# Performance work log

Hardware: AMD Instinct MI355X
Metric: run time of the kernel (lower is better)

The kernel has to match this reference:

```python
import jax, jax.numpy as jnp
import numpy as np

N_HIT = 50000
N_TRUE = 512
N_EDGE = 40000
D = 8
S_B = 1.0
Q_MIN = 0.5


def setup_inputs() -> dict:
    key = jax.random.key(0)
    k_x, k_f, k_y, k_eh, k_ep = jax.random.split(key, 5)
    x = jax.random.normal(k_x, (N_HIT, D), dtype=jnp.float32)
    # f is a sigmoid-like filter output in (0,1); keep away from 1 so atanh is finite
    f = jax.random.uniform(k_f, (N_HIT,), dtype=jnp.float32, minval=0.01, maxval=0.95)
    # y == -1 marks background hits; otherwise an instance id
    y = jax.random.randint(k_y, (N_HIT,), -1, N_TRUE, dtype=jnp.int64)
    e_h = jax.random.randint(k_eh, (N_EDGE,), 0, N_HIT, dtype=jnp.int64)
    e_p = jax.random.randint(k_ep, (N_EDGE,), 0, N_TRUE, dtype=jnp.int64)
    # guarantee every true particle has at least one assigned hit
    e_p = e_p.at[:N_TRUE].set(jnp.arange(N_TRUE, dtype=jnp.int64))
    return {"x": x, "f": f, "y": y, "e_h": e_h, "e_p": e_p}


def reference(x, f, y, e_h, e_p):
    n_hit = x.shape[0]
    fe = f[e_h]  # [n_edge]
    # scatter_max with zero-initialized output: clamp below at 0
    f_centers = jax.ops.segment_max(fe, e_p, num_segments=N_TRUE)
    f_centers = jnp.maximum(f_centers, 0.0)  # [n_true]
    # argmax hit per particle: among edges attaining the segment max, take largest hit id
    is_max = fe == f_centers[e_p]
    centers = jax.ops.segment_max(jnp.where(is_max, e_h, -1), e_p, num_segments=N_TRUE)  # [n_true]

    bkg_mask = y == -1
    n_bkg = bkg_mask.sum().astype(f.dtype)

    b1 = 1.0 - f_centers.sum() / N_TRUE
    b2 = S_B / n_bkg * jnp.where(bkg_mask, f, 0.0).sum()

    q = jnp.square(jnp.arctanh(f)) + Q_MIN  # [n_hit]

    # membership mask m_ik [n_hit, n_true]
    m_ik = jnp.zeros((n_hit, N_TRUE), dtype=bool).at[e_h, e_p].set(True)

    # pairwise squared distances to condensation centers [n_hit, n_true]
    xc = x[centers]  # [n_true, d]
    dist = jnp.sum(jnp.square(x[:, None, :] - xc[None, :, :]), axis=2)

    # attractive inside instance, hinged repulsive outside
    v = jnp.where(m_ik, dist, jnp.clip(1.0 - dist, 0.0))
    v = (jnp.sum(v * q[centers][None, :], axis=1) * q).sum() / n_hit

    return jnp.stack([b1 + b2, v])
```

## Files before the change

### kernel.cpp

```cpp
#include <hip/hip_runtime.h>
#include <math.h>

#define N_HIT  50000
#define N_TRUE 512
#define N_EDGE 40000
#define Q_MIN  0.5f

#define W_CENTERS   512
#define W_SUMFC     1024
#define W_DONE_EDGE 1025
#define W_DONE_MAIN 1026
#define W_VPART     1040
#define W_ZERO_LO   512
#define W_ZERO_HI   1168
#define W_BKGPART   1200
#define W_BKGCNT    1232
#define W_FCPART    2048
#define W_CTAB      16384
#define W_HREC      32768

#define A_EDGE_BLOCKS 16
#define A_BKG_BLOCKS  32
#define A_GRID 49
#define EPB (N_EDGE / A_EDGE_BLOCKS)

#define E_GRID ((N_EDGE + 255) / 256)

#define KSPLIT 16
#define KCH    (N_TRUE / KSPLIT)
#define HPT    4
#define HCHUNK (256 * HPT)
#define NHB    ((N_HIT + HCHUNK - 1) / HCHUNK)
#define D_DENSE (NHB * KSPLIT)
#define D_CORR  16
#define D_GRID  (D_DENSE + D_CORR)

__global__ __launch_bounds__(256) void k_prep(const float* __restrict__ x,
                                              const float* __restrict__ f,
                                              const int* __restrict__ e_h,
                                              const int* __restrict__ e_p,
                                              const int* __restrict__ y,
                                              unsigned* __restrict__ ws) {
    const int b = blockIdx.x, t = threadIdx.x;
    if (b < A_EDGE_BLOCKS) {
        __shared__ unsigned lmax[N_TRUE];
        lmax[t] = 0u; lmax[t + 256] = 0u;
        __syncthreads();
        const int e0 = b * EPB;
        for (int e = e0 + t; e < e0 + EPB; e += 256)
            atomicMax(&lmax[e_p[e]], __float_as_uint(f[e_h[e]]));
        __syncthreads();
        ws[W_FCPART + b * N_TRUE + t]       = lmax[t];
        ws[W_FCPART + b * N_TRUE + t + 256] = lmax[t + 256];
    } else if (b < A_EDGE_BLOCKS + A_BKG_BLOCKS) {
        const int bb = b - A_EDGE_BLOCKS;
        float2* hrec = (float2*)(ws + W_HREC);
        float sf = 0.f, fc = 0.f;
        for (int i = bb * 256 + t; i < N_HIT; i += A_BKG_BLOCKS * 256) {
            const float4* xp = (const float4*)(x + (size_t)i * 8);
            const float4 x0 = xp[0], x1 = xp[1];
            float xi2 = x0.x * x0.x;
            xi2 = fmaf(x0.y, x0.y, xi2); xi2 = fmaf(x0.z, x0.z, xi2);
            xi2 = fmaf(x0.w, x0.w, xi2); xi2 = fmaf(x1.x, x1.x, xi2);
            xi2 = fmaf(x1.y, x1.y, xi2); xi2 = fmaf(x1.z, x1.z, xi2);
            xi2 = fmaf(x1.w, x1.w, xi2);
            const float fi = f[i];
            const float a  = atanhf(fi);
            hrec[i] = make_float2(xi2, fmaf(a, a, Q_MIN));
            if (y[i] == -1) { sf += fi; fc += 1.f; }
        }
        for (int off = 32; off; off >>= 1) {
            sf += __shfl_down(sf, off, 64);
            fc += __shfl_down(fc, off, 64);
        }
        __shared__ float r[8];
        if ((t & 63) == 0) { r[t >> 6] = sf; r[4 + (t >> 6)] = fc; }
        __syncthreads();
        if (t == 0) {
            ((float*)ws)[W_BKGPART + bb] = r[0] + r[1] + r[2] + r[3];
            ((float*)ws)[W_BKGCNT  + bb] = r[4] + r[5] + r[6] + r[7];
        }
    } else {
        for (int w = W_ZERO_LO + t; w < W_ZERO_HI; w += 256) ws[w] = 0u;
    }
}

__global__ __launch_bounds__(256) void k_edge(const float* __restrict__ x,
                                              const float* __restrict__ f,
                                              const int* __restrict__ e_h,
                                              const int* __restrict__ e_p,
                                              unsigned* __restrict__ ws) {
    const int t = threadIdx.x;
    const int e = blockIdx.x * 256 + t;
    if (e < N_EDGE) {
        const int h = e_h[e], p = e_p[e];
        unsigned fm = 0u;
#pragma unroll
        for (int b = 0; b < A_EDGE_BLOCKS; ++b)
            fm = max(fm, ws[W_FCPART + b * N_TRUE + p]);
        if (__float_as_uint(f[h]) == fm)
            atomicMax((int*)ws + W_CENTERS + p, h);
    }
    __syncthreads();
    __shared__ int is_last;
    if (t == 0) {
        __threadfence();
        is_last = (atomicAdd(&ws[W_DONE_EDGE], 1u) == E_GRID - 1);
    }
    __syncthreads();
    if (!is_last) return;

    __threadfence();
    float local = 0.f;
    for (int p = t; p < N_TRUE; p += 256) {
        unsigned fm = 0u;
#pragma unroll
        for (int b = 0; b < A_EDGE_BLOCKS; ++b)
            fm = max(fm, ws[W_FCPART + b * N_TRUE + p]);
        local += __uint_as_float(fm);
        const int c = __hip_atomic_load((int*)ws + W_CENTERS + p,
                                        __ATOMIC_RELAXED, __HIP_MEMORY_SCOPE_AGENT);
        const float4* xp = (const float4*)(x + (size_t)c * 8);
        const float4 x0 = xp[0], x1 = xp[1];
        float ck2 = x0.x * x0.x;
        ck2 = fmaf(x0.y, x0.y, ck2); ck2 = fmaf(x0.z, x0.z, ck2);
        ck2 = fmaf(x0.w, x0.w, ck2); ck2 = fmaf(x1.x, x1.x, ck2);
        ck2 = fmaf(x1.y, x1.y, ck2); ck2 = fmaf(x1.z, x1.z, ck2);
        ck2 = fmaf(x1.w, x1.w, ck2);
        const float a = atanhf(f[c]);
        float* line = (float*)ws + W_CTAB + (size_t)p * 12;
        ((float4*)line)[0] = x0;
        ((float4*)line)[1] = x1;
        line[8] = ck2;
        line[9] = fmaf(a, a, Q_MIN);
    }
    for (int off = 32; off; off >>= 1) local += __shfl_down(local, off, 64);
    __shared__ float r[4];
    if ((t & 63) == 0) r[t >> 6] = local;
    __syncthreads();
    if (t == 0) ((float*)ws)[W_SUMFC] = r[0] + r[1] + r[2] + r[3];
}

__global__ __launch_bounds__(256, 4) void k_main(const float* __restrict__ x,
                                                 const int* __restrict__ e_h,
                                                 const int* __restrict__ e_p,
                                                 unsigned* __restrict__ ws,
                                                 float* __restrict__ out) {
    const int t = threadIdx.x;
    const int b = blockIdx.x;
    const float2* __restrict__ hrec = (const float2*)(ws + W_HREC);
    float vout = 0.f;

    if (b < D_DENSE) {
        const int hb = b >> 4;
        const int kb = b & 15;
        __shared__ float ct[KCH * 12];
        for (int w = t; w < KCH * 12; w += 256)
            ct[w] = ((const float*)ws)[W_CTAB + kb * KCH * 12 + w];
        __syncthreads();

        float4 xr0[HPT], xr1[HPT];
        float  xi2[HPT], qi[HPT], acc[HPT];
#pragma unroll
        for (int j = 0; j < HPT; ++j) {
            const int i = hb * HCHUNK + j * 256 + t;
            const bool valid = (i < N_HIT);
            const int  ic = valid ? i : 0;
            const float4* xp = (const float4*)(x + (size_t)ic * 8);
            xr0[j] = xp[0]; xr1[j] = xp[1];
            const float2 hq = hrec[ic];
            xi2[j] = hq.x;
            qi[j]  = valid ? hq.y : 0.f;
            acc[j] = 0.f;
        }
#pragma unroll
        for (int k2 = 0; k2 < KCH; ++k2) {
            const float4 c0  = *(const float4*)(ct + 12 * k2);
            const float4 c1  = *(const float4*)(ct + 12 * k2 + 4);
            const float  ck2 = ct[12 * k2 + 8];
            const float  qck = ct[12 * k2 + 9];
#pragma unroll
            for (int j = 0; j < HPT; ++j) {
                float dot = xr0[j].x * c0.x;
                dot = fmaf(xr0[j].y, c0.y, dot); dot = fmaf(xr0[j].z, c0.z, dot);
                dot = fmaf(xr0[j].w, c0.w, dot); dot = fmaf(xr1[j].x, c1.x, dot);
                dot = fmaf(xr1[j].y, c1.y, dot); dot = fmaf(xr1[j].z, c1.z, dot);
                dot = fmaf(xr1[j].w, c1.w, dot);
                const float dist = fmaf(-2.f, dot, xi2[j] + ck2);
                const float rep  = fmaxf(1.f - dist, 0.f);
                acc[j] = fmaf(rep, qck, acc[j]);
            }
        }
#pragma unroll
        for (int j = 0; j < HPT; ++j) vout = fmaf(acc[j], qi[j], vout);
    } else {
        const int cb = b - D_DENSE;
        const float* __restrict__ ctab = (const float*)ws + W_CTAB;
        for (int e = cb * 256 + t; e < N_EDGE; e += D_CORR * 256) {
            const int h = e_h[e], p = e_p[e];
            const float2 hq = hrec[h];
            const float4* xp = (const float4*)(x + (size_t)h * 8);
            const float4 a0 = xp[0], a1 = xp[1];
            const float* line = ctab + (size_t)p * 12;
            const float4 c0 = *(const float4*)line;
            const float4 c1 = *(const float4*)(line + 4);
            const float ck2 = line[8], qck = line[9];
            float dot = a0.x * c0.x;
            dot = fmaf(a0.y, c0.y, dot); dot = fmaf(a0.z, c0.z, dot);
            dot = fmaf(a0.w, c0.w, dot); dot = fmaf(a1.x, c1.x, dot);
            dot = fmaf(a1.y, c1.y, dot); dot = fmaf(a1.z, c1.z, dot);
            dot = fmaf(a1.w, c1.w, dot);
            const float dist  = fmaf(-2.f, dot, hq.x + ck2);
            const float hinge = fmaxf(1.f - dist, 0.f);
            vout = fmaf(hq.y * qck, dist - hinge, vout);
        }
    }

    for (int off = 32; off; off >>= 1) vout += __shfl_down(vout, off, 64);
    __shared__ float r[4];
    if ((t & 63) == 0) r[t >> 6] = vout;
    __syncthreads();
    if (t == 0) {
        atomicAdd((float*)ws + W_VPART + (b & 7) * 16, r[0] + r[1] + r[2] + r[3]);
        __threadfence();
        const unsigned c = atomicAdd(&ws[W_DONE_MAIN], 1u);
        if (c == D_GRID - 1) {
            __threadfence();
            float vs = 0.f;
            for (int s = 0; s < 8; ++s)
                vs += atomicAdd((float*)ws + W_VPART + s * 16, 0.0f);
            float sum_bkg = 0.f, nb = 0.f;
            for (int s = 0; s < A_BKG_BLOCKS; ++s) {
                sum_bkg += __hip_atomic_load((const float*)ws + W_BKGPART + s,
                                             __ATOMIC_RELAXED, __HIP_MEMORY_SCOPE_AGENT);
                nb      += __hip_atomic_load((const float*)ws + W_BKGCNT + s,
                                             __ATOMIC_RELAXED, __HIP_MEMORY_SCOPE_AGENT);
            }
            const float sum_fc = __hip_atomic_load((const float*)ws + W_SUMFC,
                                                   __ATOMIC_RELAXED, __HIP_MEMORY_SCOPE_AGENT);
            out[0] = (1.f - sum_fc / (float)N_TRUE) + sum_bkg / nb;
            out[1] = vs / (float)N_HIT;
        }
    }
}

extern "C" void kernel_launch(void* const* d_in, const int* in_sizes, int n_in,
                              void* d_out, int out_size, void* d_ws, size_t ws_size,
                              hipStream_t stream) {
    const float* x   = (const float*)d_in[0];
    const float* f   = (const float*)d_in[1];
    const int*   y   = (const int*)d_in[2];
    const int*   e_h = (const int*)d_in[3];
    const int*   e_p = (const int*)d_in[4];
    float* out = (float*)d_out;
    unsigned* ws = (unsigned*)d_ws;

    k_prep<<<A_GRID, 256, 0, stream>>>(x, f, e_h, e_p, y, ws);
    k_edge<<<E_GRID, 256, 0, stream>>>(x, f, e_h, e_p, ws);
    k_main<<<D_GRID, 256, 0, stream>>>(x, e_h, e_p, ws, out);
}
```

Measured before the change: 104.9 us.

## Fuse prep, edge and main kernels into one persistent kernel with grid barrier

Replaces the three-kernel pipeline with a tiny init kernel plus one fused kernel of 800 blocks. The segment max and argmax are computed in one pass by packing the float bits and the hit id into a 64-bit atomicMax. The prep phase is separated from the dense phase by a software grid barrier that spins on an arrival counter. The aim is to remove kernel launch gaps and the separate argmax pass, but the barrier only works if all 800 blocks are resident at once, and the edge correction now gathers center data per edge from x and hrec.

Result: slower. 263.3 us (+150.9%).

```diff
diff --git a/kernel.cpp b/kernel.cpp
--- a/kernel.cpp
+++ b/kernel.cpp
@@ -6,57 +6,50 @@
 #define N_EDGE 40000
 #define Q_MIN  0.5f
 
-#define W_CENTERS   512
-#define W_SUMFC     1024
-#define W_DONE_EDGE 1025
-#define W_DONE_MAIN 1026
-#define W_VPART     1040
-#define W_ZERO_LO   512
-#define W_ZERO_HI   1168
-#define W_BKGPART   1200
-#define W_BKGCNT    1232
-#define W_FCPART    2048
-#define W_CTAB      16384
-#define W_HREC      32768
-
-#define A_EDGE_BLOCKS 16
-#define A_BKG_BLOCKS  32
-#define A_GRID 49
-#define EPB (N_EDGE / A_EDGE_BLOCKS)
-
-#define E_GRID ((N_EDGE + 255) / 256)
-
-#define KSPLIT 16
-#define KCH    (N_TRUE / KSPLIT)
-#define HPT    4
-#define HCHUNK (256 * HPT)
-#define NHB    ((N_HIT + HCHUNK - 1) / HCHUNK)
-#define D_DENSE (NHB * KSPLIT)
-#define D_CORR  16
-#define D_GRID  (D_DENSE + D_CORR)
-
-__global__ __launch_bounds__(256) void k_prep(const float* __restrict__ x,
-                                              const float* __restrict__ f,
-                                              const int* __restrict__ e_h,
-                                              const int* __restrict__ e_p,
-                                              const int* __restrict__ y,
-                                              unsigned* __restrict__ ws) {
-    const int b = blockIdx.x, t = threadIdx.x;
-    if (b < A_EDGE_BLOCKS) {
-        __shared__ unsigned lmax[N_TRUE];
-        lmax[t] = 0u; lmax[t + 256] = 0u;
-        __syncthreads();
-        const int e0 = b * EPB;
-        for (int e = e0 + t; e < e0 + EPB; e += 256)
-            atomicMax(&lmax[e_p[e]], __float_as_uint(f[e_h[e]]));
-        __syncthreads();
-        ws[W_FCPART + b * N_TRUE + t]       = lmax[t];
-        ws[W_FCPART + b * N_TRUE + t + 256] = lmax[t + 256];
-    } else if (b < A_EDGE_BLOCKS + A_BKG_BLOCKS) {
-        const int bb = b - A_EDGE_BLOCKS;
-        float2* hrec = (float2*)(ws + W_HREC);
-        float sf = 0.f, fc = 0.f;
-        for (int i = bb * 256 + t; i < N_HIT; i += A_BKG_BLOCKS * 256) {
+#define W_SEG     0
+#define W_ARRIVE  1024
+#define W_DONE    1025
+#define W_SUMFC   1026
+#define W_SUMBKG  1027
+#define W_NBKG    1028
+#define W_VPART   1040
+#define W_ZERO_HI 1168
+#define W_HREC    2048
+
+#define G_BLOCKS  800
+#define EPB       (N_EDGE / G_BLOCKS)
+#define KSPLIT    16
+#define KCH       (N_TRUE / KSPLIT)
+#define HPT       4
+#define HCHUNK    (256 * HPT)
+
+__global__ __launch_bounds__(256) void k_init(unsigned* __restrict__ ws) {
+    for (int w = threadIdx.x; w < W_ZERO_HI; w += 256) ws[w] = 0u;
+}
+
+__global__ __launch_bounds__(256, 4) void k_fused(const float* __restrict__ x,
+                                                  const float* __restrict__ f,
+                                                  const int* __restrict__ y,
+                                                  const int* __restrict__ e_h,
+                                                  const int* __restrict__ e_p,
+                                                  unsigned* __restrict__ ws,
+                                                  float* __restrict__ out) {
+    const int t = threadIdx.x, b = blockIdx.x;
+    unsigned long long* __restrict__ seg = (unsigned long long*)ws;
+    float2* __restrict__ hrec = (float2*)(ws + W_HREC);
+
+    if (t >= 64 && t < 64 + EPB) {
+        const int e = b * EPB + (t - 64);
+        const int h = e_h[e], p = e_p[e];
+        const unsigned long long packed =
+            ((unsigned long long)__float_as_uint(f[h]) << 32) | (unsigned)h;
+        atomicMax(&seg[p], packed);
+    }
+    if (t < 64) {
+        const int i = b * 64 + t;
+        float sf = 0.f;
+        bool isb = false;
+        if (i < N_HIT) {
             const float4* xp = (const float4*)(x + (size_t)i * 8);
             const float4 x0 = xp[0], x1 = xp[1];
             float xi2 = x0.x * x0.x;
@@ -67,178 +60,127 @@
             const float fi = f[i];
             const float a  = atanhf(fi);
             hrec[i] = make_float2(xi2, fmaf(a, a, Q_MIN));
-            if (y[i] == -1) { sf += fi; fc += 1.f; }
-        }
-        for (int off = 32; off; off >>= 1) {
-            sf += __shfl_down(sf, off, 64);
-            fc += __shfl_down(fc, off, 64);
-        }
-        __shared__ float r[8];
-        if ((t & 63) == 0) { r[t >> 6] = sf; r[4 + (t >> 6)] = fc; }
+            isb = (y[i] == -1);
+            if (isb) sf = fi;
+        }
+        for (int off = 32; off; off >>= 1) sf += __shfl_down(sf, off, 64);
+        const unsigned long long bal = __ballot(isb);
+        if (t == 0) {
+            atomicAdd((float*)ws + W_SUMBKG, sf);
+            atomicAdd(&ws[W_NBKG], (unsigned)__popcll(bal));
+        }
+    }
+
+    __threadfence();
+    __syncthreads();
+    if (t == 0) {
+        atomicAdd(&ws[W_ARRIVE], 1u);
+        while (__hip_atomic_load(&ws[W_ARRIVE], __ATOMIC_ACQUIRE,
+                                 __HIP_MEMORY_SCOPE_AGENT) < (unsigned)G_BLOCKS)
+            __builtin_amdgcn_s_sleep(2);
+    }
+    __syncthreads();
+    __threadfence();
+
+    __shared__ float ct[KCH * 12];
+    __shared__ float r[4];
+    const int kb = b & (KSPLIT - 1);
+    const int hb = b >> 4;
+    if (t < KCH) {
+        const unsigned long long w = seg[kb * KCH + t];
+        const int c = (int)(unsigned)w;
+        const float4* xp = (const float4*)(x + (size_t)c * 8);
+        const float2 hc = hrec[c];
+        *(float4*)(ct + 12 * t)     = xp[0];
+        *(float4*)(ct + 12 * t + 4) = xp[1];
+        ct[12 * t + 8] = hc.x;
+        ct[12 * t + 9] = hc.y;
+    }
+    if (b == 0) {
+        float lc = __uint_as_float((unsigned)(seg[t] >> 32)) +
+                   __uint_as_float((unsigned)(seg[t + 256] >> 32));
+        for (int off = 32; off; off >>= 1) lc += __shfl_down(lc, off, 64);
+        if ((t & 63) == 0) r[t >> 6] = lc;
         __syncthreads();
-        if (t == 0) {
-            ((float*)ws)[W_BKGPART + bb] = r[0] + r[1] + r[2] + r[3];
-            ((float*)ws)[W_BKGCNT  + bb] = r[4] + r[5] + r[6] + r[7];
-        }
-    } else {
-        for (int w = W_ZERO_LO + t; w < W_ZERO_HI; w += 256) ws[w] = 0u;
-    }
-}
-
-__global__ __launch_bounds__(256) void k_edge(const float* __restrict__ x,
-                                              const float* __restrict__ f,
-                                              const int* __restrict__ e_h,
-                                              const int* __restrict__ e_p,
-                                              unsigned* __restrict__ ws) {
-    const int t = threadIdx.x;
-    const int e = blockIdx.x * 256 + t;
-    if (e < N_EDGE) {
+        if (t == 0) ((float*)ws)[W_SUMFC] = r[0] + r[1] + r[2] + r[3];
+    }
+    __syncthreads();
+
+    float4 xr0[HPT], xr1[HPT];
+    float  xi2v[HPT], qiv[HPT], acc[HPT];
+#pragma unroll
+    for (int j = 0; j < HPT; ++j) {
+        const int i = hb * HCHUNK + j * 256 + t;
+        const bool valid = (i < N_HIT);
+        const int  ic = valid ? i : 0;
+        const float4* xp = (const float4*)(x + (size_t)ic * 8);
+        xr0[j] = xp[0]; xr1[j] = xp[1];
+        const float2 hq = hrec[ic];
+        xi2v[j] = hq.x;
+        qiv[j]  = valid ? hq.y : 0.f;
+        acc[j]  = 0.f;
+    }
+#pragma unroll
+    for (int k2 = 0; k2 < KCH; ++k2) {
+        const float4 c0  = *(const float4*)(ct + 12 * k2);
+        const float4 c1  = *(const float4*)(ct + 12 * k2 + 4);
+        const float  ck2 = ct[12 * k2 + 8];
+        const float  qck = ct[12 * k2 + 9];
+#pragma unroll
+        for (int j = 0; j < HPT; ++j) {
+            float dot = xr0[j].x * c0.x;
+            dot = fmaf(xr0[j].y, c0.y, dot); dot = fmaf(xr0[j].z, c0.z, dot);
+            dot = fmaf(xr0[j].w, c0.w, dot); dot = fmaf(xr1[j].x, c1.x, dot);
+            dot = fmaf(xr1[j].y, c1.y, dot); dot = fmaf(xr1[j].z, c1.z, dot);
+            dot = fmaf(xr1[j].w, c1.w, dot);
+            const float dist = fmaf(-2.f, dot, xi2v[j] + ck2);
+            const float rep  = fmaxf(1.f - dist, 0.f);
+            acc[j] = fmaf(rep, qck, acc[j]);
+        }
+    }
+    float vout = 0.f;
+#pragma unroll
+    for (int j = 0; j < HPT; ++j) vout = fmaf(acc[j], qiv[j], vout);
+
+    if (t < EPB) {
+        const int e = b * EPB + t;
         const int h = e_h[e], p = e_p[e];
-        unsigned fm = 0u;
-#pragma unroll
-        for (int b = 0; b < A_EDGE_BLOCKS; ++b)
-            fm = max(fm, ws[W_FCPART + b * N_TRUE + p]);
-        if (__float_as_uint(f[h]) == fm)
-            atomicMax((int*)ws + W_CENTERS + p, h);
-    }
-    __syncthreads();
-    __shared__ int is_last;
-    if (t == 0) {
-        __threadfence();
-        is_last = (atomicAdd(&ws[W_DONE_EDGE], 1u) == E_GRID - 1);
-    }
-    __syncthreads();
-    if (!is_last) return;
-
-    __threadfence();
-    float local = 0.f;
-    for (int p = t; p < N_TRUE; p += 256) {
-        unsigned fm = 0u;
-#pragma unroll
-        for (int b = 0; b < A_EDGE_BLOCKS; ++b)
-            fm = max(fm, ws[W_FCPART + b * N_TRUE + p]);
-        local += __uint_as_float(fm);
-        const int c = __hip_atomic_load((int*)ws + W_CENTERS + p,
-                                        __ATOMIC_RELAXED, __HIP_MEMORY_SCOPE_AGENT);
-        const float4* xp = (const float4*)(x + (size_t)c * 8);
-        const float4 x0 = xp[0], x1 = xp[1];
-        float ck2 = x0.x * x0.x;
-        ck2 = fmaf(x0.y, x0.y, ck2); ck2 = fmaf(x0.z, x0.z, ck2);
-        ck2 = fmaf(x0.w, x0.w, ck2); ck2 = fmaf(x1.x, x1.x, ck2);
-        ck2 = fmaf(x1.y, x1.y, ck2); ck2 = fmaf(x1.z, x1.z, ck2);
-        ck2 = fmaf(x1.w, x1.w, ck2);
-        const float a = atanhf(f[c]);
-        float* line = (float*)ws + W_CTAB + (size_t)p * 12;
-        ((float4*)line)[0] = x0;
-        ((float4*)line)[1] = x1;
-        line[8] = ck2;
-        line[9] = fmaf(a, a, Q_MIN);
-    }
-    for (int off = 32; off; off >>= 1) local += __shfl_down(local, off, 64);
-    __shared__ float r[4];
-    if ((t & 63) == 0) r[t >> 6] = local;
-    __syncthreads();
-    if (t == 0) ((float*)ws)[W_SUMFC] = r[0] + r[1] + r[2] + r[3];
-}
-
-__global__ __launch_bounds__(256, 4) void k_main(const float* __restrict__ x,
-                                                 const int* __restrict__ e_h,
-                                                 const int* __restrict__ e_p,
-                                                 unsigned* __restrict__ ws,
-                                                 float* __restrict__ out) {
-    const int t = threadIdx.x;
-    const int b = blockIdx.x;
-    const float2* __restrict__ hrec = (const float2*)(ws + W_HREC);
-    float vout = 0.f;
-
-    if (b < D_DENSE) {
-        const int hb = b >> 4;
-        const int kb = b & 15;
-        __shared__ float ct[KCH * 12];
-        for (int w = t; w < KCH * 12; w += 256)
-            ct[w] = ((const float*)ws)[W_CTAB + kb * KCH * 12 + w];
-        __syncthreads();
-
-        float4 xr0[HPT], xr1[HPT];
-        float  xi2[HPT], qi[HPT], acc[HPT];
-#pragma unroll
-        for (int j = 0; j < HPT; ++j) {
-            const int i = hb * HCHUNK + j * 256 + t;
-            const bool valid = (i < N_HIT);
-            const int  ic = valid ? i : 0;
-            const float4* xp = (const float4*)(x + (size_t)ic * 8);
-            xr0[j] = xp[0]; xr1[j] = xp[1];
-            const float2 hq = hrec[ic];
-            xi2[j] = hq.x;
-            qi[j]  = valid ? hq.y : 0.f;
-            acc[j] = 0.f;
-        }
-#pragma unroll
-        for (int k2 = 0; k2 < KCH; ++k2) {
-            const float4 c0  = *(const float4*)(ct + 12 * k2);
-            const float4 c1  = *(const float4*)(ct + 12 * k2 + 4);
-            const float  ck2 = ct[12 * k2 + 8];
-            const float  qck = ct[12 * k2 + 9];
-#pragma unroll
-            for (int j = 0; j < HPT; ++j) {
-                float dot = xr0[j].x * c0.x;
-                dot = fmaf(xr0[j].y, c0.y, dot); dot = fmaf(xr0[j].z, c0.z, dot);
-                dot = fmaf(xr0[j].w, c0.w, dot); dot = fmaf(xr1[j].x, c1.x, dot);
-                dot = fmaf(xr1[j].y, c1.y, dot); dot = fmaf(xr1[j].z, c1.z, dot);
-                dot = fmaf(xr1[j].w, c1.w, dot);
-                const float dist = fmaf(-2.f, dot, xi2[j] + ck2);
-                const float rep  = fmaxf(1.f - dist, 0.f);
-                acc[j] = fmaf(rep, qck, acc[j]);
-            }
-        }
-#pragma unroll
-        for (int j = 0; j < HPT; ++j) vout = fmaf(acc[j], qi[j], vout);
-    } else {
-        const int cb = b - D_DENSE;
-        const float* __restrict__ ctab = (const float*)ws + W_CTAB;
-        for (int e = cb * 256 + t; e < N_EDGE; e += D_CORR * 256) {
-            const int h = e_h[e], p = e_p[e];
-            const float2 hq = hrec[h];
-            const float4* xp = (const float4*)(x + (size_t)h * 8);
-            const float4 a0 = xp[0], a1 = xp[1];
-            const float* line = ctab + (size_t)p * 12;
-            const float4 c0 = *(const float4*)line;
-            const float4 c1 = *(const float4*)(line + 4);
-            const float ck2 = line[8], qck = line[9];
-            float dot = a0.x * c0.x;
-            dot = fmaf(a0.y, c0.y, dot); dot = fmaf(a0.z, c0.z, dot);
-            dot = fmaf(a0.w, c0.w, dot); dot = fmaf(a1.x, c1.x, dot);
-            dot = fmaf(a1.y, c1.y, dot); dot = fmaf(a1.z, c1.z, dot);
-            dot = fmaf(a1.w, c1.w, dot);
-            const float dist  = fmaf(-2.f, dot, hq.x + ck2);
-            const float hinge = fmaxf(1.f - dist, 0.f);
-            vout = fmaf(hq.y * qck, dist - hinge, vout);
-        }
+        const unsigned long long w = seg[p];
+        const int c = (int)(unsigned)w;
+        const float4* hp4 = (const float4*)(x + (size_t)h * 8);
+        const float4 a0 = hp4[0], a1 = hp4[1];
+        const float4* cp4 = (const float4*)(x + (size_t)c * 8);
+        const float4 c0 = cp4[0], c1 = cp4[1];
+        const float2 hh = hrec[h], hc = hrec[c];
+        float dot = a0.x * c0.x;
+        dot = fmaf(a0.y, c0.y, dot); dot = fmaf(a0.z, c0.z, dot);
+        dot = fmaf(a0.w, c0.w, dot); dot = fmaf(a1.x, c1.x, dot);
+        dot = fmaf(a1.y, c1.y, dot); dot = fmaf(a1.z, c1.z, dot);
+        dot = fmaf(a1.w, c1.w, dot);
+        const float dist  = fmaf(-2.f, dot, hh.x + hc.x);
+        const float hinge = fmaxf(1.f - dist, 0.f);
+        vout = fmaf(hh.y * hc.y, dist - hinge, vout);
     }
 
     for (int off = 32; off; off >>= 1) vout += __shfl_down(vout, off, 64);
-    __shared__ float r[4];
     if ((t & 63) == 0) r[t >> 6] = vout;
     __syncthreads();
     if (t == 0) {
         atomicAdd((float*)ws + W_VPART + (b & 7) * 16, r[0] + r[1] + r[2] + r[3]);
         __threadfence();
-        const unsigned c = atomicAdd(&ws[W_DONE_MAIN], 1u);
-        if (c == D_GRID - 1) {
+        const unsigned c = atomicAdd(&ws[W_DONE], 1u);
+        if (c == G_BLOCKS - 1) {
             __threadfence();
             float vs = 0.f;
             for (int s = 0; s < 8; ++s)
                 vs += atomicAdd((float*)ws + W_VPART + s * 16, 0.0f);
-            float sum_bkg = 0.f, nb = 0.f;
-            for (int s = 0; s < A_BKG_BLOCKS; ++s) {
-                sum_bkg += __hip_atomic_load((const float*)ws + W_BKGPART + s,
-                                             __ATOMIC_RELAXED, __HIP_MEMORY_SCOPE_AGENT);
-                nb      += __hip_atomic_load((const float*)ws + W_BKGCNT + s,
-                                             __ATOMIC_RELAXED, __HIP_MEMORY_SCOPE_AGENT);
-            }
-            const float sum_fc = __hip_atomic_load((const float*)ws + W_SUMFC,
-                                                   __ATOMIC_RELAXED, __HIP_MEMORY_SCOPE_AGENT);
-            out[0] = (1.f - sum_fc / (float)N_TRUE) + sum_bkg / nb;
+            const float sum_bkg = __hip_atomic_load((const float*)ws + W_SUMBKG,
+                                                    __ATOMIC_RELAXED, __HIP_MEMORY_SCOPE_AGENT);
+            const float sum_fc  = __hip_atomic_load((const float*)ws + W_SUMFC,
+                                                    __ATOMIC_RELAXED, __HIP_MEMORY_SCOPE_AGENT);
+            const unsigned nb   = __hip_atomic_load(&ws[W_NBKG],
+                                                    __ATOMIC_RELAXED, __HIP_MEMORY_SCOPE_AGENT);
+            out[0] = (1.f - sum_fc / (float)N_TRUE) + sum_bkg / (float)nb;
             out[1] = vs / (float)N_HIT;
         }
     }
@@ -255,7 +197,6 @@
     float* out = (float*)d_out;
     unsigned* ws = (unsigned*)d_ws;
 
-    k_prep<<<A_GRID, 256, 0, stream>>>(x, f, e_h, e_p, y, ws);
-    k_edge<<<E_GRID, 256, 0, stream>>>(x, f, e_h, e_p, ws);
-    k_main<<<D_GRID, 256, 0, stream>>>(x, e_h, e_p, ws, out);
+    k_init<<<1, 256, 0, stream>>>(ws);
+    k_fused<<<G_BLOCKS, 256, 0, stream>>>(x, f, y, e_h, e_p, ws, out);
 }
```
